# Performance work log

Hardware: AMD Instinct MI355X
Metric: run time of the kernel (lower is better)

## Reference

```python
import jax, jax.numpy as jnp
import numpy as np

N_CLASSES = 16
N_CATEGORY = 4096
OUT = 512
BS = 4096


def setup_inputs() -> dict:
    key = jax.random.key(0)
    k1, k2, k3 = jax.random.split(key, 3)
    batch = jax.random.normal(k1, (BS, N_CATEGORY), dtype=jnp.float32)
    classes = jax.random.randint(k2, (BS,), 0, N_CLASSES, dtype=jnp.int32)
    # Stacked per-class Linear weights, each [out, in] like nn.Linear.weight.
    W = jax.random.normal(k3, (N_CLASSES, OUT, N_CATEGORY), dtype=jnp.float32) * 0.02
    return {"batch": batch, "classes": classes, "W": W}


def reference(batch, classes, W):
    # Original: result[i] = W[classes[i]] @ batch[i]  (per-sample class-indexed linear).
    # Vectorized: compute all experts' outputs [b, c, o], then select per-sample class.
    all_out = jnp.einsum('bi,coi->bco', batch, W)
    out = jnp.take_along_axis(all_out, classes.astype(jnp.int32)[:, None, None], axis=1)
    return out[:, 0, :]  # [bs, out]
```

## Files before the change

### kernel.cpp

```cpp
#include <hip/hip_runtime.h>
#include <hip/hip_bf16.h>

typedef __attribute__((ext_vector_type(4))) float f32x4;
typedef __attribute__((ext_vector_type(8))) short s16x8;

#define NCLS 16
#define NCAT 4096
#define NOUT 512
#define NBS  4096

#define BM 128
#define BN 128
#define BK 64
#define NSPLIT 4
#define KSPLIT (NCAT / NSPLIT)
#define NITER  (KSPLIT / BK)
#define MAXTILES 48

#define WS_NT    0
#define WS_CBASE 1
#define WS_TCLS  32
#define WS_TM0   96
#define WS_SIDX  160

__global__ __launch_bounds__(256) void prep_kernel(const int* __restrict__ cls,
                                                   int* __restrict__ ws) {
  __shared__ int lcnt[NCLS * 256];
  __shared__ int cb[NCLS];
  __shared__ int ctot[NCLS];
  const int t = threadIdx.x;

  int cl[16];
  #pragma unroll
  for (int j = 0; j < 16; ++j) cl[j] = cls[j * 256 + t];

  int cnt[NCLS];
  #pragma unroll
  for (int c = 0; c < NCLS; ++c) cnt[c] = 0;
  #pragma unroll
  for (int j = 0; j < 16; ++j) {
    #pragma unroll
    for (int c = 0; c < NCLS; ++c) cnt[c] += (cl[j] == c) ? 1 : 0;
  }
  #pragma unroll
  for (int c = 0; c < NCLS; ++c) lcnt[c * 256 + t] = cnt[c];
  __syncthreads();

  if (t < NCLS) {
    int run = 0;
    for (int u = 0; u < 256; ++u) {
      int v = lcnt[t * 256 + u];
      lcnt[t * 256 + u] = run;
      run += v;
    }
    ctot[t] = run;
  }
  __syncthreads();

  if (t == 0) {
    int acc = 0, nt_ = 0;
    for (int c = 0; c < NCLS; ++c) {
      cb[c] = acc;
      ws[WS_CBASE + c] = acc;
      for (int m0 = 0; m0 < ctot[c]; m0 += BM) {
        ws[WS_TCLS + nt_] = c;
        ws[WS_TM0 + nt_] = m0;
        ++nt_;
      }
      acc += ctot[c];
    }
    ws[WS_CBASE + NCLS] = acc;
    ws[WS_NT] = nt_;
  }
  __syncthreads();

  #pragma unroll
  for (int j = 0; j < 16; ++j) {
    int c = cl[j];
    int within = 0;
    #pragma unroll
    for (int j2 = 0; j2 < 16; ++j2) within += (j2 < j && cl[j2] == c) ? 1 : 0;
    ws[WS_SIDX + cb[c] + lcnt[c * 256 + t] + within] = j * 256 + t;
  }
}

__device__ __forceinline__ void pk2(float x0, float x1, unsigned& hb, unsigned& lb) {
  __hip_bfloat162 h2 = __float22bfloat162_rn(make_float2(x0, x1));
  float2 hf = __bfloat1622float2(h2);
  __hip_bfloat162 l2 = __float22bfloat162_rn(make_float2(x0 - hf.x, x1 - hf.y));
  __builtin_memcpy(&hb, &h2, 4);
  __builtin_memcpy(&lb, &l2, 4);
}

__device__ __forceinline__ void cvt8(float4 a, float4 b, uint4& hi, uint4& lo) {
  pk2(a.x, a.y, hi.x, lo.x);
  pk2(a.z, a.w, hi.y, lo.y);
  pk2(b.x, b.y, hi.z, lo.z);
  pk2(b.z, b.w, hi.w, lo.w);
}

__global__ __launch_bounds__(256, 2) void gemm_kernel(const float* __restrict__ batch,
                                                      const float* __restrict__ W,
                                                      const int* __restrict__ ws,
                                                      float* __restrict__ out) {
  const int tile = blockIdx.x;
  if (tile >= ws[WS_NT]) return;
  const int c    = ws[WS_TCLS + tile];
  const int m0   = ws[WS_TM0 + tile];
  const int base = ws[WS_CBASE + c];
  const int Mc   = ws[WS_CBASE + c + 1] - base;
  const int n0   = blockIdx.y * BN;
  const int k0   = blockIdx.z * KSPLIT;
  const int* sidx = ws + WS_SIDX + base;

  __shared__ char lds[4 * BM * BK * 2];
  char* const Ahi = lds;
  char* const Alo = lds + 16384;
  char* const Bhi = lds + 32768;
  char* const Blo = lds + 49152;

  const int t = threadIdx.x;
  const int r = t >> 1;
  const int h = t & 1;
  const int arow = sidx[min(m0 + r, Mc - 1)];
  const float* aptr = batch + (size_t)arow * NCAT + k0 + h * 32;
  const float* bptr = W + ((size_t)c * NOUT + (n0 + r)) * NCAT + k0 + h * 32;
  const int wswz = (r & 7) << 4;

  const int lane = t & 63;
  const int wv   = t >> 6;
  const int wm   = (wv >> 1) * 64;
  const int wn   = (wv & 1) * 64;
  const int l15  = lane & 15;
  const int kg16 = (lane >> 4) * 16;

  f32x4 acc[4][4];
  #pragma unroll
  for (int i = 0; i < 4; ++i)
    #pragma unroll
    for (int j = 0; j < 4; ++j) acc[i][j] = (f32x4){0.f, 0.f, 0.f, 0.f};

  float4 pa0[4], pa1[4], pb0[4], pb1[4];
  #pragma unroll
  for (int cc = 0; cc < 4; ++cc) {
    const int ko = cc * 8;
    pa0[cc] = *(const float4*)(aptr + ko);
    pa1[cc] = *(const float4*)(aptr + ko + 4);
    pb0[cc] = *(const float4*)(bptr + ko);
    pb1[cc] = *(const float4*)(bptr + ko + 4);
  }

  for (int it = 0; it < NITER; ++it) {
    __syncthreads();
    #pragma unroll
    for (int cc = 0; cc < 4; ++cc) {
      uint4 ah, al, bh, bl;
      cvt8(pa0[cc], pa1[cc], ah, al);
      cvt8(pb0[cc], pb1[cc], bh, bl);
      const int off = r * 128 + ((h * 64 + cc * 16) ^ wswz);
      *(uint4*)(Ahi + off) = ah;
      *(uint4*)(Alo + off) = al;
      *(uint4*)(Bhi + off) = bh;
      *(uint4*)(Blo + off) = bl;
    }
    if (it + 1 < NITER) {
      const int kt = (it + 1) * BK;
      #pragma unroll
      for (int cc = 0; cc < 4; ++cc) {
        const int ko = kt + cc * 8;
        pa0[cc] = *(const float4*)(aptr + ko);
        pa1[cc] = *(const float4*)(aptr + ko + 4);
        pb0[cc] = *(const float4*)(bptr + ko);
        pb1[cc] = *(const float4*)(bptr + ko + 4);
      }
    }
    __syncthreads();
    #pragma unroll
    for (int ks = 0; ks < 2; ++ks) {
      s16x8 ahf[4], alf[4], bhf[4], blf[4];
      #pragma unroll
      for (int i = 0; i < 4; ++i) {
        const int m = wm + i * 16 + l15;
        const int offa = m * 128 + ((ks * 64 + kg16) ^ ((m & 7) << 4));
        ahf[i] = *(const s16x8*)(Ahi + offa);
        alf[i] = *(const s16x8*)(Alo + offa);
        const int n = wn + i * 16 + l15;
        const int offb = n * 128 + ((ks * 64 + kg16) ^ ((n & 7) << 4));
        bhf[i] = *(const s16x8*)(Bhi + offb);
        blf[i] = *(const s16x8*)(Blo + offb);
      }
      #pragma unroll
      for (int i = 0; i < 4; ++i)
        #pragma unroll
        for (int j = 0; j < 4; ++j) {
          acc[i][j] = __builtin_amdgcn_mfma_f32_16x16x32_bf16(ahf[i], bhf[j], acc[i][j], 0, 0, 0);
          acc[i][j] = __builtin_amdgcn_mfma_f32_16x16x32_bf16(ahf[i], blf[j], acc[i][j], 0, 0, 0);
          acc[i][j] = __builtin_amdgcn_mfma_f32_16x16x32_bf16(alf[i], bhf[j], acc[i][j], 0, 0, 0);
        }
    }
  }

  const int r4 = (lane >> 4) * 4;
  #pragma unroll
  for (int i = 0; i < 4; ++i) {
    #pragma unroll
    for (int jj = 0; jj < 4; ++jj) {
      const int mloc = wm + i * 16 + r4 + jj;
      const int gm = m0 + mloc;
      if (gm < Mc) {
        const int sample = sidx[gm];
        float* orow = out + (size_t)sample * NOUT + n0 + wn;
        #pragma unroll
        for (int j = 0; j < 4; ++j) {
          atomicAdd(orow + j * 16 + l15, acc[i][j][jj]);
        }
      }
    }
  }
}

extern "C" void kernel_launch(void* const* d_in, const int* in_sizes, int n_in,
                              void* d_out, int out_size, void* d_ws, size_t ws_size,
                              hipStream_t stream) {
  const float* batch = (const float*)d_in[0];
  const int*   cls   = (const int*)d_in[1];
  const float* W     = (const float*)d_in[2];
  float* out = (float*)d_out;
  int*   ws  = (int*)d_ws;

  prep_kernel<<<1, 256, 0, stream>>>(cls, ws);
  hipMemsetAsync(d_out, 0, (size_t)out_size * sizeof(float), stream);
  gemm_kernel<<<dim3(MAXTILES, NOUT / BN, NSPLIT), 256, 0, stream>>>(batch, W, ws, out);
}
```

Measured before the change: 365.8 us.

## Stream fp32 tiles to LDS via async global_load_lds with double buffering

Replaces the register-staged load, bf16 hi/lo split and LDS store with direct global-to-LDS async loads of raw fp32 tiles (BK reduced to 32), double-buffered and synchronized with vmcnt waits and barriers. The bf16 split now happens after reading from LDS, so each wave converts its own fragments. This removes register staging and VGPR pressure from the load path and overlaps memory with MFMA. In exchange, conversion work is redundant across waves that share fragments and there are more barrier iterations. The prep kernel's serial per-class prefix sum is also replaced by a parallel Hillis-Steele scan.

After: 314.5 us. -14.0%, faster.

```diff
diff --git a/kernel.cpp b/kernel.cpp
--- a/kernel.cpp
+++ b/kernel.cpp
@@ -11,10 +11,10 @@
 
 #define BM 128
 #define BN 128
-#define BK 64
+#define BK 32
 #define NSPLIT 4
 #define KSPLIT (NCAT / NSPLIT)
-#define NITER  (KSPLIT / BK)
+#define NIT    (KSPLIT / BK)
 #define MAXTILES 48
 
 #define WS_NT    0
@@ -27,7 +27,6 @@
                                                    int* __restrict__ ws) {
   __shared__ int lcnt[NCLS * 256];
   __shared__ int cb[NCLS];
-  __shared__ int ctot[NCLS];
   const int t = threadIdx.x;
 
   int cl[16];
@@ -46,31 +45,31 @@
   for (int c = 0; c < NCLS; ++c) lcnt[c * 256 + t] = cnt[c];
   __syncthreads();
 
-  if (t < NCLS) {
-    int run = 0;
-    for (int u = 0; u < 256; ++u) {
-      int v = lcnt[t * 256 + u];
-      lcnt[t * 256 + u] = run;
-      run += v;
-    }
-    ctot[t] = run;
-  }
-  __syncthreads();
+  for (int d = 1; d < 256; d <<= 1) {
+    int add[NCLS];
+    #pragma unroll
+    for (int c = 0; c < NCLS; ++c) add[c] = (t >= d) ? lcnt[c * 256 + t - d] : 0;
+    __syncthreads();
+    #pragma unroll
+    for (int c = 0; c < NCLS; ++c) if (t >= d) lcnt[c * 256 + t] += add[c];
+    __syncthreads();
+  }
 
   if (t == 0) {
-    int acc = 0, nt_ = 0;
+    int acc = 0, ntt = 0;
     for (int c = 0; c < NCLS; ++c) {
       cb[c] = acc;
       ws[WS_CBASE + c] = acc;
-      for (int m0 = 0; m0 < ctot[c]; m0 += BM) {
-        ws[WS_TCLS + nt_] = c;
-        ws[WS_TM0 + nt_] = m0;
-        ++nt_;
-      }
-      acc += ctot[c];
+      int tot = lcnt[c * 256 + 255];
+      for (int m0 = 0; m0 < tot; m0 += BM) {
+        ws[WS_TCLS + ntt] = c;
+        ws[WS_TM0 + ntt] = m0;
+        ++ntt;
+      }
+      acc += tot;
     }
     ws[WS_CBASE + NCLS] = acc;
-    ws[WS_NT] = nt_;
+    ws[WS_NT] = ntt;
   }
   __syncthreads();
 
@@ -80,8 +79,15 @@
     int within = 0;
     #pragma unroll
     for (int j2 = 0; j2 < 16; ++j2) within += (j2 < j && cl[j2] == c) ? 1 : 0;
-    ws[WS_SIDX + cb[c] + lcnt[c * 256 + t] + within] = j * 256 + t;
-  }
+    ws[WS_SIDX + cb[c] + (lcnt[c * 256 + t] - cnt[c]) + within] = j * 256 + t;
+  }
+}
+
+typedef const __attribute__((address_space(1))) void* gas_ptr;
+typedef __attribute__((address_space(3))) void* las_ptr;
+
+__device__ __forceinline__ void gl_lds16(const void* g, void* l) {
+  __builtin_amdgcn_global_load_lds((gas_ptr)g, (las_ptr)l, 16, 0, 0);
 }
 
 __device__ __forceinline__ void pk2(float x0, float x1, unsigned& hb, unsigned& lb) {
@@ -92,11 +98,13 @@
   __builtin_memcpy(&lb, &l2, 4);
 }
 
-__device__ __forceinline__ void cvt8(float4 a, float4 b, uint4& hi, uint4& lo) {
-  pk2(a.x, a.y, hi.x, lo.x);
-  pk2(a.z, a.w, hi.y, lo.y);
-  pk2(b.x, b.y, hi.z, lo.z);
-  pk2(b.z, b.w, hi.w, lo.w);
+__device__ __forceinline__ void cvt8(f32x4 p, f32x4 q, s16x8& hi, s16x8& lo) {
+  union { s16x8 v; unsigned u[4]; } H, L;
+  pk2(p[0], p[1], H.u[0], L.u[0]);
+  pk2(p[2], p[3], H.u[1], L.u[1]);
+  pk2(q[0], q[1], H.u[2], L.u[2]);
+  pk2(q[2], q[3], H.u[3], L.u[3]);
+  hi = H.v; lo = L.v;
 }
 
 __global__ __launch_bounds__(256, 2) void gemm_kernel(const float* __restrict__ batch,
@@ -113,26 +121,31 @@
   const int k0   = blockIdx.z * KSPLIT;
   const int* sidx = ws + WS_SIDX + base;
 
-  __shared__ char lds[4 * BM * BK * 2];
-  char* const Ahi = lds;
-  char* const Alo = lds + 16384;
-  char* const Bhi = lds + 32768;
-  char* const Blo = lds + 49152;
-
-  const int t = threadIdx.x;
-  const int r = t >> 1;
-  const int h = t & 1;
-  const int arow = sidx[min(m0 + r, Mc - 1)];
-  const float* aptr = batch + (size_t)arow * NCAT + k0 + h * 32;
-  const float* bptr = W + ((size_t)c * NOUT + (n0 + r)) * NCAT + k0 + h * 32;
-  const int wswz = (r & 7) << 4;
-
+  __shared__ char lds[65536];
+
+  const int t    = threadIdx.x;
   const int lane = t & 63;
   const int wv   = t >> 6;
-  const int wm   = (wv >> 1) * 64;
-  const int wn   = (wv & 1) * 64;
   const int l15  = lane & 15;
-  const int kg16 = (lane >> 4) * 16;
+
+  const int rsub = lane >> 3;
+  const int ko   = (((lane & 7) ^ rsub) << 4);
+  const char* aga[4];
+  const char* bga[4];
+  #pragma unroll
+  for (int j = 0; j < 4; ++j) {
+    const int rr = 32 * wv + 8 * j + rsub;
+    const int ar = sidx[min(m0 + rr, Mc - 1)];
+    aga[j] = (const char*)batch + ((size_t)ar * NCAT + k0) * 4 + ko;
+    const int br = c * NOUT + n0 + rr;
+    bga[j] = (const char*)W + ((size_t)br * NCAT + k0) * 4 + ko;
+  }
+
+  char* const stA = lds + (32 * wv) * 128;
+
+  const int wm  = (wv >> 1) * 64;
+  const int wn  = (wv & 1) * 64;
+  const int kb0 = (lane >> 4) * 32;
 
   f32x4 acc[4][4];
   #pragma unroll
@@ -140,63 +153,61 @@
     #pragma unroll
     for (int j = 0; j < 4; ++j) acc[i][j] = (f32x4){0.f, 0.f, 0.f, 0.f};
 
-  float4 pa0[4], pa1[4], pb0[4], pb1[4];
-  #pragma unroll
-  for (int cc = 0; cc < 4; ++cc) {
-    const int ko = cc * 8;
-    pa0[cc] = *(const float4*)(aptr + ko);
-    pa1[cc] = *(const float4*)(aptr + ko + 4);
-    pb0[cc] = *(const float4*)(bptr + ko);
-    pb1[cc] = *(const float4*)(bptr + ko + 4);
-  }
-
-  for (int it = 0; it < NITER; ++it) {
-    __syncthreads();
-    #pragma unroll
-    for (int cc = 0; cc < 4; ++cc) {
-      uint4 ah, al, bh, bl;
-      cvt8(pa0[cc], pa1[cc], ah, al);
-      cvt8(pb0[cc], pb1[cc], bh, bl);
-      const int off = r * 128 + ((h * 64 + cc * 16) ^ wswz);
-      *(uint4*)(Ahi + off) = ah;
-      *(uint4*)(Alo + off) = al;
-      *(uint4*)(Bhi + off) = bh;
-      *(uint4*)(Blo + off) = bl;
-    }
-    if (it + 1 < NITER) {
-      const int kt = (it + 1) * BK;
-      #pragma unroll
-      for (int cc = 0; cc < 4; ++cc) {
-        const int ko = kt + cc * 8;
-        pa0[cc] = *(const float4*)(aptr + ko);
-        pa1[cc] = *(const float4*)(aptr + ko + 4);
-        pb0[cc] = *(const float4*)(bptr + ko);
-        pb1[cc] = *(const float4*)(bptr + ko + 4);
-      }
-    }
-    __syncthreads();
-    #pragma unroll
-    for (int ks = 0; ks < 2; ++ks) {
-      s16x8 ahf[4], alf[4], bhf[4], blf[4];
+  #pragma unroll
+  for (int j = 0; j < 4; ++j) {
+    gl_lds16(aga[j] + 0 * 128, stA + j * 1024);
+    gl_lds16(bga[j] + 0 * 128, stA + 16384 + j * 1024);
+  }
+  #pragma unroll
+  for (int j = 0; j < 4; ++j) {
+    gl_lds16(aga[j] + 1 * 128, stA + 32768 + j * 1024);
+    gl_lds16(bga[j] + 1 * 128, stA + 32768 + 16384 + j * 1024);
+  }
+
+  for (int it = 0; it < NIT; ++it) {
+    if (it < NIT - 1) asm volatile("s_waitcnt vmcnt(8)" ::: "memory");
+    else              asm volatile("s_waitcnt vmcnt(0)" ::: "memory");
+    __builtin_amdgcn_s_barrier();
+    asm volatile("" ::: "memory");
+
+    {
+      const char* const bufp = lds + (it & 1) * 32768;
+      s16x8 Ah[4], Al[4], Bh[4], Bl[4];
       #pragma unroll
       for (int i = 0; i < 4; ++i) {
         const int m = wm + i * 16 + l15;
-        const int offa = m * 128 + ((ks * 64 + kg16) ^ ((m & 7) << 4));
-        ahf[i] = *(const s16x8*)(Ahi + offa);
-        alf[i] = *(const s16x8*)(Alo + offa);
+        const char* rowp = bufp + m * 128;
+        const int swzm = (m & 7) << 4;
+        f32x4 p = *(const f32x4*)(rowp + ((kb0) ^ swzm));
+        f32x4 q = *(const f32x4*)(rowp + ((kb0 + 16) ^ swzm));
+        cvt8(p, q, Ah[i], Al[i]);
         const int n = wn + i * 16 + l15;
-        const int offb = n * 128 + ((ks * 64 + kg16) ^ ((n & 7) << 4));
-        bhf[i] = *(const s16x8*)(Bhi + offb);
-        blf[i] = *(const s16x8*)(Blo + offb);
+        const char* rowq = bufp + 16384 + n * 128;
+        const int swzn = (n & 7) << 4;
+        f32x4 r = *(const f32x4*)(rowq + ((kb0) ^ swzn));
+        f32x4 s = *(const f32x4*)(rowq + ((kb0 + 16) ^ swzn));
+        cvt8(r, s, Bh[i], Bl[i]);
       }
       #pragma unroll
       for (int i = 0; i < 4; ++i)
         #pragma unroll
         for (int j = 0; j < 4; ++j) {
-          acc[i][j] = __builtin_amdgcn_mfma_f32_16x16x32_bf16(ahf[i], bhf[j], acc[i][j], 0, 0, 0);
-          acc[i][j] = __builtin_amdgcn_mfma_f32_16x16x32_bf16(ahf[i], blf[j], acc[i][j], 0, 0, 0);
-          acc[i][j] = __builtin_amdgcn_mfma_f32_16x16x32_bf16(alf[i], bhf[j], acc[i][j], 0, 0, 0);
+          acc[i][j] = __builtin_amdgcn_mfma_f32_16x16x32_bf16(Ah[i], Bh[j], acc[i][j], 0, 0, 0);
+          acc[i][j] = __builtin_amdgcn_mfma_f32_16x16x32_bf16(Ah[i], Bl[j], acc[i][j], 0, 0, 0);
+          acc[i][j] = __builtin_amdgcn_mfma_f32_16x16x32_bf16(Al[i], Bh[j], acc[i][j], 0, 0, 0);
         }
+    }
+
+    asm volatile("" ::: "memory");
+    __builtin_amdgcn_s_barrier();
+    if (it + 2 < NIT) {
+      char* const dst = lds + (it & 1) * 32768 + (32 * wv) * 128;
+      const int koff = (it + 2) * 128;
+      #pragma unroll
+      for (int j = 0; j < 4; ++j) {
+        gl_lds16(aga[j] + koff, dst + j * 1024);
+        gl_lds16(bga[j] + koff, dst + 16384 + j * 1024);
+      }
     }
   }
 
```
